# Optimization experiments

Hardware: AMD Instinct MI355X
Metric: run time of the kernel (lower is better)

Reference implementation:

```python
import jax, jax.numpy as jnp
import numpy as np

B, NV, NH = 65536, 16, 16


def _tri(key, b, n, scale=0.1):
    # well-conditioned lower-triangular 'cholesky-like' factor: unit diagonal + small strict-lower part
    a = jax.random.normal(key, (b, n, n), dtype=jnp.float32) * scale
    return jnp.tril(a, -1) + jnp.eye(n, dtype=jnp.float32)[None, :, :]


def setup_inputs() -> dict:
    key = jax.random.key(0)
    ks = jax.random.split(key, 9)
    # SPD, well-conditioned precision matrix for the hidden block
    a = jax.random.normal(ks[0], (B, NH, NH), dtype=jnp.float32)
    prec_h = jnp.eye(NH, dtype=jnp.float32)[None, :, :] + 0.1 * jnp.matmul(a, jnp.swapaxes(a, -1, -2)) / NH
    return {
        'mu_TE': jax.random.normal(ks[1], (B, NV + NH), dtype=jnp.float32),
        'prec_h': prec_h,
        'chol_v': _tri(ks[2], B, NV),
        'chol_h': _tri(ks[3], B, NH),
        'chol_hv': jax.random.normal(ks[4], (B, NH, NV), dtype=jnp.float32) * 0.1,
        'chol_v_TE': jax.random.normal(ks[5], (B, NV, NV), dtype=jnp.float32) * 0.1,
        'chol_h_TE': jax.random.normal(ks[6], (B, NH, NH), dtype=jnp.float32) * 0.1,
        'chol_hv_TE': jax.random.normal(ks[7], (B, NH, NV), dtype=jnp.float32) * 0.1,
        'chol_amat': _tri(ks[8], B, NV),
        'nv': NV,
    }


def reference(mu_TE, prec_h, chol_v, chol_h, chol_hv, chol_v_TE, chol_h_TE, chol_hv_TE, chol_amat, nv):
    T = lambda m: jnp.swapaxes(m, -1, -2)
    prec_h_inv = jnp.linalg.inv(prec_h)  # [B,nh,nh]

    # d/dt of prec_h_inv via product rule on chol factors
    sym = (chol_h_TE @ T(chol_h) + chol_h @ T(chol_h_TE)
           + chol_hv_TE @ T(chol_hv) + chol_hv @ T(chol_hv_TE))
    prec_h_inv_TE = -(prec_h_inv @ sym @ prec_h_inv)

    # amat_TE = -d/dt [ chol_hv^T prec_h_inv chol_hv ]  -> [B,nv,nv]
    amat_TE = -(T(chol_hv_TE) @ (prec_h_inv @ chol_hv)
                + T(chol_hv) @ (prec_h_inv_TE @ chol_hv)
                + T(chol_hv) @ (prec_h_inv @ chol_hv_TE))

    # make_chol_mat_TE: Phi(L^-1 A L^-T) keeps strict lower triangle + half diagonal
    n = chol_amat.shape[-1]
    phi_mask = jnp.tril(jnp.ones((n, n), jnp.float32), -1) + 0.5 * jnp.eye(n, dtype=jnp.float32)
    cinv = jnp.linalg.inv(chol_amat)
    arg = cinv @ amat_TE @ T(cinv)
    chol_amat_TE = chol_amat @ (arg * phi_mask)

    cholv_TE_std = chol_v_TE @ chol_amat + chol_v @ chol_amat_TE
    muv_TE = mu_TE[:, :nv]
    return cholv_TE_std, muv_TE
```

## Files before the change

kernel.cpp:

```cpp
#include <hip/hip_runtime.h>


typedef _Float16 h2 __attribute__((ext_vector_type(2)));

constexpr int PITCH = 20;
constexpr int IMG   = 8 * PITCH;
constexpr int NSLOT = 5;
constexpr int BSTR  = NSLOT * IMG + 8;

#define WBAR() __builtin_amdgcn_wave_barrier()

__device__ __forceinline__ unsigned int pkf(float a, float b) {
  return __builtin_bit_cast(unsigned int, __builtin_amdgcn_cvt_pkrtz(a, b));
}
__device__ __forceinline__ unsigned int h2add(unsigned int a, unsigned int b) {
  return __builtin_bit_cast(unsigned int,
      (h2)(__builtin_bit_cast(h2, a) + __builtin_bit_cast(h2, b)));
}
__device__ __forceinline__ float fd2(unsigned int a, unsigned int b, float c) {
#if __has_builtin(__builtin_amdgcn_fdot2)
  return __builtin_amdgcn_fdot2(__builtin_bit_cast(h2, a), __builtin_bit_cast(h2, b), c, false);
#else
  h2 ha = __builtin_bit_cast(h2, a), hb = __builtin_bit_cast(h2, b);
  return c + (float)ha.x * (float)hb.x + (float)ha.y * (float)hb.y;
#endif
}
__device__ __forceinline__ float dpp_swap1(float v) {
  return __int_as_float(__builtin_amdgcn_update_dpp(
      0, __float_as_int(v), 0xB1, 0xF, 0xF, false));
}

__device__ __forceinline__ void zero16(float (&v)[16]) {
  #pragma unroll
  for (int j = 0; j < 16; ++j) v[j] = 0.f;
}

__device__ __forceinline__ void ldtile(const float* __restrict__ g, size_t batch,
                                       int p, int q, float (&c)[16]) {
  const float* base = g + batch * 256 + p * 64 + q * 4;
  #pragma unroll
  for (int r = 0; r < 4; ++r) {
    float4 v = *reinterpret_cast<const float4*>(base + r * 16);
    c[r*4+0] = v.x; c[r*4+1] = v.y; c[r*4+2] = v.z; c[r*4+3] = v.w;
  }
}

__device__ __forceinline__ void storeRP(unsigned int* img, int p, int q, const float (&c)[16]) {
  #pragma unroll
  for (int r = 0; r < 4; ++r) {
    img[(2*q  ) * PITCH + 4*p + r] = pkf(c[r*4+0], c[r*4+1]);
    img[(2*q+1) * PITCH + 4*p + r] = pkf(c[r*4+2], c[r*4+3]);
  }
}
__device__ __forceinline__ void packCP(const float (&c)[16], unsigned int (&w)[8]) {
  w[0] = pkf(c[0],  c[4]);  w[1] = pkf(c[1],  c[5]);
  w[2] = pkf(c[2],  c[6]);  w[3] = pkf(c[3],  c[7]);
  w[4] = pkf(c[8],  c[12]); w[5] = pkf(c[9],  c[13]);
  w[6] = pkf(c[10], c[14]); w[7] = pkf(c[11], c[15]);
}
__device__ __forceinline__ void writeCPregs(unsigned int* img, int p, int q,
                                            const unsigned int (&w)[8]) {
  *reinterpret_cast<uint4*>(img + (2*p  ) * PITCH + 4*q) = make_uint4(w[0], w[1], w[2], w[3]);
  *reinterpret_cast<uint4*>(img + (2*p+1) * PITCH + 4*q) = make_uint4(w[4], w[5], w[6], w[7]);
}
__device__ __forceinline__ void storeCP(unsigned int* img, int p, int q, const float (&c)[16]) {
  unsigned int w[8];
  packCP(c, w);
  writeCPregs(img, p, q, w);
}

__device__ __forceinline__ void mm1(const unsigned int* __restrict__ A,
                                    const unsigned int* __restrict__ Bm,
                                    int p4, int q4, float (&c)[16]) {
  #pragma unroll
  for (int kp = 0; kp < 8; ++kp) {
    uint4 av = *reinterpret_cast<const uint4*>(A  + kp * PITCH + p4);
    uint4 bv = *reinterpret_cast<const uint4*>(Bm + kp * PITCH + q4);
    const unsigned int ar[4] = {av.x, av.y, av.z, av.w};
    const unsigned int br[4] = {bv.x, bv.y, bv.z, bv.w};
    #pragma unroll
    for (int r = 0; r < 4; ++r)
      #pragma unroll
      for (int j = 0; j < 4; ++j)
        c[r*4+j] = fd2(ar[r], br[j], c[r*4+j]);
  }
}
__device__ __forceinline__ void mm2(const unsigned int* __restrict__ A0,
                                    const unsigned int* __restrict__ A1,
                                    const unsigned int* __restrict__ Bm,
                                    int p4, int q4, float (&c)[16]) {
  #pragma unroll
  for (int kp = 0; kp < 8; ++kp) {
    uint4 a0 = *reinterpret_cast<const uint4*>(A0 + kp * PITCH + p4);
    uint4 a1 = *reinterpret_cast<const uint4*>(A1 + kp * PITCH + p4);
    uint4 bv = *reinterpret_cast<const uint4*>(Bm + kp * PITCH + q4);
    const unsigned int ar[4] = {h2add(a0.x, a1.x), h2add(a0.y, a1.y),
                                h2add(a0.z, a1.z), h2add(a0.w, a1.w)};
    const unsigned int br[4] = {bv.x, bv.y, bv.z, bv.w};
    #pragma unroll
    for (int r = 0; r < 4; ++r)
      #pragma unroll
      for (int j = 0; j < 4; ++j)
        c[r*4+j] = fd2(ar[r], br[j], c[r*4+j]);
  }
}

__global__ __launch_bounds__(64, 3) void gauss_te_pk5(
    const float* __restrict__ mu_TE,
    const float* __restrict__ prec_h,
    const float* __restrict__ chol_v,
    const float* __restrict__ chol_h,
    const float* __restrict__ chol_hv,
    const float* __restrict__ chol_v_TE,
    const float* __restrict__ chol_h_TE,
    const float* __restrict__ chol_hv_TE,
    const float* __restrict__ chol_amat,
    float* __restrict__ out, int B)
{
  __shared__ __align__(16) unsigned int slab[4 * BSTR];
  const int t = threadIdx.x;
  const int g = t >> 4;
  const int l = t & 15;
  const int p = l >> 2, q = l & 3;
  const int p4 = 4 * p, q4 = 4 * q;
  const size_t batch = (size_t)blockIdx.x * 4 + g;

  unsigned int* U = slab + g * BSTR;
  unsigned int* P0 = U;            unsigned int* P1 = U + 1*IMG;
  unsigned int* P2 = U + 2*IMG;    unsigned int* P3 = U + 3*IMG;
  unsigned int* P4 = U + 4*IMG;
  float* fcol = reinterpret_cast<float*>(P1);
  float* brow = fcol + 32;

  out[(size_t)B * 256 + batch * 16 + l] = mu_TE[batch * 32 + l];

  float tt[16];
  ldtile(chol_h, batch, p, q, tt);     storeRP(P0, p, q, tt);
  ldtile(chol_h_TE, batch, p, q, tt);  storeRP(P1, p, q, tt);
  unsigned int cphv[8], cphvT[8];
  ldtile(chol_hv, batch, p, q, tt);    storeRP(P2, p, q, tt);  packCP(tt, cphv);
  ldtile(chol_hv_TE, batch, p, q, tt); storeRP(P3, p, q, tt);  packCP(tt, cphvT);
  float pt[16];
  ldtile(prec_h, batch, p, q, pt);
  float la[16];
  ldtile(chol_amat, batch, p, q, la);
  WBAR();

  float c[16];

  zero16(c);
  mm1(P1, P0, p4, q4, c);
  mm1(P3, P2, p4, q4, c);
  storeCP(P4, c != nullptr ? p : p, q, c);
  WBAR();
  writeCPregs(P2, p, q, cphv);
  writeCPregs(P3, p, q, cphvT);
  WBAR();

  #pragma unroll
  for (int k = 0; k < 16; ++k) {
    const int kb = k >> 2, kc = k & 3, sel = (k & 1) * 16;
    if (q == kb) {
      *reinterpret_cast<float4*>(fcol + sel + p4) =
          make_float4(pt[0*4+kc], pt[1*4+kc], pt[2*4+kc], pt[3*4+kc]);
    }
    WBAR();
    if (p == kb) {
      const float rinv = 1.0f / fcol[sel + k];
      float sv[4];
      #pragma unroll
      for (int j = 0; j < 4; ++j) sv[j] = pt[kc*4+j] * rinv;
      if (q == kb) sv[kc] = rinv;
      *reinterpret_cast<float4*>(brow + sel + q4) = make_float4(sv[0], sv[1], sv[2], sv[3]);
    }
    WBAR();
    float4 f4 = *reinterpret_cast<const float4*>(fcol + sel + p4);
    float4 b4 = *reinterpret_cast<const float4*>(brow + sel + q4);
    const float fr[4] = {f4.x, f4.y, f4.z, f4.w};
    const float br[4] = {b4.x, b4.y, b4.z, b4.w};
    #pragma unroll
    for (int r = 0; r < 4; ++r) {
      const bool isPivRow = (p == kb) && (r == kc);
      #pragma unroll
      for (int j = 0; j < 4; ++j) {
        float base = pt[r*4+j];
        if (q == kb && j == kc) base = 0.f;
        const float nv = base - fr[r] * br[j];
        pt[r*4+j] = isPivRow ? br[j] : nv;
      }
    }
  }
  WBAR();
  storeRP(P0, p, q, pt);
  WBAR();

  zero16(c);
  mm1(P0, P4, p4, q4, c);
  WBAR();
  storeRP(P1, p, q, c);
  WBAR();

  zero16(c);
  mm1(P1, P0, p4, q4, c);
  WBAR();
  storeRP(P4, p, q, c);
  storeCP(P1, p, q, c);
  WBAR();

  zero16(c);
  mm1(P0, P2, p4, q4, c);
  WBAR();
  storeCP(P0, p, q, c);
  WBAR();

  zero16(c);
  mm2(P4, P1, P2, p4, q4, c);
  WBAR();
  storeCP(P4, p, q, c);
  WBAR();

  zero16(c);
  mm1(P3, P0, p4, q4, c);
  const int srcT = (t & 48) | ((t & 3) << 2) | ((t >> 2) & 3);
  float zsum[16];
  #pragma unroll
  for (int r = 0; r < 4; ++r)
    #pragma unroll
    for (int j = 0; j < 4; ++j)
      zsum[r*4+j] = c[r*4+j] + __shfl(c[j*4+r], srcT, 64);
  WBAR();

  zero16(c);
  mm1(P2, P4, p4, q4, c);
  #pragma unroll
  for (int j = 0; j < 16; ++j) c[j] -= zsum[j];
  WBAR();
  storeRP(P0, p, q, c);
  storeCP(P1, p, q, la);
  storeRP(P3, p, q, la);
  WBAR();

  float x[16];
  #pragma unroll
  for (int kp = 0; kp < 8; ++kp) {
    const int r0 = 2 * kp, r1 = r0 + 1;
    float a0 = 0.f, a1 = 0.f, h10 = 0.f;
    #pragma unroll
    for (int c2 = 0; c2 <= kp / 2; ++c2) {
      uint4 cv = *reinterpret_cast<const uint4*>(P1 + kp * PITCH + 4 * c2);
      const unsigned int cw[4] = {cv.x, cv.y, cv.z, cv.w};
      #pragma unroll
      for (int cc = 0; cc < 4; ++cc) {
        const int j = 4 * c2 + cc;
        h2 hp = __builtin_bit_cast(h2, cw[cc]);
        if (j < r0) a0 = fmaf(-(float)hp.x, x[j], a0);
        if (j < r0) a1 = fmaf(-(float)hp.y, x[j], a1);
        if (j == r0) h10 = (float)hp.y;
      }
    }
    x[r0] = ((l == r0) ? 1.f : 0.f) + a0;
    x[r1] = ((l == r1) ? 1.f : 0.f) + a1 - h10 * x[r0];
  }
  {
    float xp[16];
    #pragma unroll
    for (int j = 0; j < 16; ++j) xp[j] = dpp_swap1(x[j]);
    if ((l & 1) == 0) {
      unsigned int* dst = P2 + (l >> 1) * PITCH;
      #pragma unroll
      for (int c4 = 0; c4 < 4; ++c4) {
        uint4 w;
        w.x = pkf(x[4*c4+0], xp[4*c4+0]); w.y = pkf(x[4*c4+1], xp[4*c4+1]);
        w.z = pkf(x[4*c4+2], xp[4*c4+2]); w.w = pkf(x[4*c4+3], xp[4*c4+3]);
        *reinterpret_cast<uint4*>(dst + 4*c4) = w;
      }
    }
  }
  WBAR();

  float lvt[16], lv[16];
  ldtile(chol_v_TE, batch, p, q, lvt);
  ldtile(chol_v, batch, p, q, lv);

  zero16(c);
  mm1(P0, P2, p4, q4, c);
  WBAR();
  storeCP(P4, p, q, c);
  WBAR();

  zero16(c);
  mm1(P2, P4, p4, q4, c);
  #pragma unroll
  for (int r = 0; r < 4; ++r)
    #pragma unroll
    for (int j = 0; j < 4; ++j) {
      const int gi = p4 + r, gj = q4 + j;
      c[r*4+j] = (gi > gj) ? c[r*4+j] : ((gi == gj) ? 0.5f * c[r*4+j] : 0.f);
    }
  WBAR();
  storeCP(P0, p, q, c);
  WBAR();

  zero16(c);
  mm1(P3, P0, p4, q4, c);
  WBAR();
  storeCP(P4, p, q, c);
  storeRP(P0, p, q, lvt);
  storeRP(P2, p, q, lv);
  WBAR();

  zero16(c);
  mm1(P0, P1, p4, q4, c);
  mm1(P2, P4, p4, q4, c);
  {
    float* base = out + batch * 256 + p * 64 + q * 4;
    #pragma unroll
    for (int r = 0; r < 4; ++r)
      *reinterpret_cast<float4*>(base + r * 16) =
          make_float4(c[r*4+0], c[r*4+1], c[r*4+2], c[r*4+3]);
  }
}

extern "C" void kernel_launch(void* const* d_in, const int* in_sizes, int n_in,
                              void* d_out, int out_size, void* d_ws, size_t ws_size,
                              hipStream_t stream) {
  const float* mu_TE      = (const float*)d_in[0];
  const float* prec_h     = (const float*)d_in[1];
  const float* chol_v     = (const float*)d_in[2];
  const float* chol_h     = (const float*)d_in[3];
  const float* chol_hv    = (const float*)d_in[4];
  const float* chol_v_TE  = (const float*)d_in[5];
  const float* chol_h_TE  = (const float*)d_in[6];
  const float* chol_hv_TE = (const float*)d_in[7];
  const float* chol_amat  = (const float*)d_in[8];
  float* out = (float*)d_out;

  const int B = in_sizes[0] / 32;
  gauss_te_pk5<<<B / 4, 64, 0, stream>>>(mu_TE, prec_h, chol_v, chol_h, chol_hv,
                                         chol_v_TE, chol_h_TE, chol_hv_TE,
                                         chol_amat, out, B);
}
```

Before: 131.9 us.

## Replace fdot2 matrix products with 16x16x16 f16 MFMA across whole wave

The per-batch 16x16 matrix products, previously done by 16-lane groups with packed fdot2 on LDS images, now run as wave-wide 16x16x16 f16 MFMA instructions. Two batches are processed per pass, and several operands are loaded and converted straight from global memory. The algebra is also reassociated (P^-1 S P^-1, then a symmetric sum) so fewer LDS slots are needed. LDS per block shrinks from five slots to four and launch bounds rise to four blocks, aiming at higher occupancy and less ALU work, at the cost of more uncoalesced column loads and lane-layout shuffles.

```diff
diff --git a/kernel.cpp b/kernel.cpp
--- a/kernel.cpp
+++ b/kernel.cpp
@@ -1,38 +1,34 @@
 #include <hip/hip_runtime.h>
 
 
-typedef _Float16 h2 __attribute__((ext_vector_type(2)));
+typedef _Float16 h2    __attribute__((ext_vector_type(2)));
+typedef _Float16 f16x4 __attribute__((ext_vector_type(4)));
+typedef float    f32x4 __attribute__((ext_vector_type(4)));
 
 constexpr int PITCH = 20;
 constexpr int IMG   = 8 * PITCH;
-constexpr int NSLOT = 5;
-constexpr int BSTR  = NSLOT * IMG + 8;
+constexpr int BSTR  = 4 * IMG + 8;
 
 #define WBAR() __builtin_amdgcn_wave_barrier()
 
 __device__ __forceinline__ unsigned int pkf(float a, float b) {
   return __builtin_bit_cast(unsigned int, __builtin_amdgcn_cvt_pkrtz(a, b));
 }
-__device__ __forceinline__ unsigned int h2add(unsigned int a, unsigned int b) {
-  return __builtin_bit_cast(unsigned int,
-      (h2)(__builtin_bit_cast(h2, a) + __builtin_bit_cast(h2, b)));
-}
-__device__ __forceinline__ float fd2(unsigned int a, unsigned int b, float c) {
-#if __has_builtin(__builtin_amdgcn_fdot2)
-  return __builtin_amdgcn_fdot2(__builtin_bit_cast(h2, a), __builtin_bit_cast(h2, b), c, false);
-#else
-  h2 ha = __builtin_bit_cast(h2, a), hb = __builtin_bit_cast(h2, b);
-  return c + (float)ha.x * (float)hb.x + (float)ha.y * (float)hb.y;
-#endif
+__device__ __forceinline__ f16x4 mkf16x4(unsigned int lo, unsigned int hi) {
+  union { unsigned int u[2]; f16x4 v; } cv; cv.u[0] = lo; cv.u[1] = hi; return cv.v;
+}
+__device__ __forceinline__ f16x4 cvt4(f32x4 d) {
+  return mkf16x4(pkf(d[0], d[1]), pkf(d[2], d[3]));
+}
+__device__ __forceinline__ f16x4 cvt4f(float a, float b, float c, float d) {
+  return mkf16x4(pkf(a, b), pkf(c, d));
 }
 __device__ __forceinline__ float dpp_swap1(float v) {
   return __int_as_float(__builtin_amdgcn_update_dpp(
       0, __float_as_int(v), 0xB1, 0xF, 0xF, false));
 }
-
-__device__ __forceinline__ void zero16(float (&v)[16]) {
-  #pragma unroll
-  for (int j = 0; j < 16; ++j) v[j] = 0.f;
+__device__ __forceinline__ f32x4 MF(f16x4 a, f16x4 b, f32x4 c) {
+  return __builtin_amdgcn_mfma_f32_16x16x16f16(a, b, c, 0, 0, 0);
 }
 
 __device__ __forceinline__ void ldtile(const float* __restrict__ g, size_t batch,
@@ -44,7 +40,6 @@
     c[r*4+0] = v.x; c[r*4+1] = v.y; c[r*4+2] = v.z; c[r*4+3] = v.w;
   }
 }
-
 __device__ __forceinline__ void storeRP(unsigned int* img, int p, int q, const float (&c)[16]) {
   #pragma unroll
   for (int r = 0; r < 4; ++r) {
@@ -52,60 +47,39 @@
     img[(2*q+1) * PITCH + 4*p + r] = pkf(c[r*4+2], c[r*4+3]);
   }
 }
-__device__ __forceinline__ void packCP(const float (&c)[16], unsigned int (&w)[8]) {
-  w[0] = pkf(c[0],  c[4]);  w[1] = pkf(c[1],  c[5]);
-  w[2] = pkf(c[2],  c[6]);  w[3] = pkf(c[3],  c[7]);
-  w[4] = pkf(c[8],  c[12]); w[5] = pkf(c[9],  c[13]);
-  w[6] = pkf(c[10], c[14]); w[7] = pkf(c[11], c[15]);
-}
-__device__ __forceinline__ void writeCPregs(unsigned int* img, int p, int q,
-                                            const unsigned int (&w)[8]) {
-  *reinterpret_cast<uint4*>(img + (2*p  ) * PITCH + 4*q) = make_uint4(w[0], w[1], w[2], w[3]);
-  *reinterpret_cast<uint4*>(img + (2*p+1) * PITCH + 4*q) = make_uint4(w[4], w[5], w[6], w[7]);
-}
-__device__ __forceinline__ void storeCP(unsigned int* img, int p, int q, const float (&c)[16]) {
-  unsigned int w[8];
-  packCP(c, w);
-  writeCPregs(img, p, q, w);
-}
-
-__device__ __forceinline__ void mm1(const unsigned int* __restrict__ A,
-                                    const unsigned int* __restrict__ Bm,
-                                    int p4, int q4, float (&c)[16]) {
-  #pragma unroll
-  for (int kp = 0; kp < 8; ++kp) {
-    uint4 av = *reinterpret_cast<const uint4*>(A  + kp * PITCH + p4);
-    uint4 bv = *reinterpret_cast<const uint4*>(Bm + kp * PITCH + q4);
-    const unsigned int ar[4] = {av.x, av.y, av.z, av.w};
-    const unsigned int br[4] = {bv.x, bv.y, bv.z, bv.w};
-    #pragma unroll
-    for (int r = 0; r < 4; ++r)
-      #pragma unroll
-      for (int j = 0; j < 4; ++j)
-        c[r*4+j] = fd2(ar[r], br[j], c[r*4+j]);
-  }
-}
-__device__ __forceinline__ void mm2(const unsigned int* __restrict__ A0,
-                                    const unsigned int* __restrict__ A1,
-                                    const unsigned int* __restrict__ Bm,
-                                    int p4, int q4, float (&c)[16]) {
-  #pragma unroll
-  for (int kp = 0; kp < 8; ++kp) {
-    uint4 a0 = *reinterpret_cast<const uint4*>(A0 + kp * PITCH + p4);
-    uint4 a1 = *reinterpret_cast<const uint4*>(A1 + kp * PITCH + p4);
-    uint4 bv = *reinterpret_cast<const uint4*>(Bm + kp * PITCH + q4);
-    const unsigned int ar[4] = {h2add(a0.x, a1.x), h2add(a0.y, a1.y),
-                                h2add(a0.z, a1.z), h2add(a0.w, a1.w)};
-    const unsigned int br[4] = {bv.x, bv.y, bv.z, bv.w};
-    #pragma unroll
-    for (int r = 0; r < 4; ++r)
-      #pragma unroll
-      for (int j = 0; j < 4; ++j)
-        c[r*4+j] = fd2(ar[r], br[j], c[r*4+j]);
-  }
-}
-
-__global__ __launch_bounds__(64, 3) void gauss_te_pk5(
+__device__ __forceinline__ void storeCPt(unsigned int* img, int p, int q, const float (&c)[16]) {
+  uint4 w0, w1;
+  w0.x = pkf(c[0],  c[4]);  w0.y = pkf(c[1],  c[5]);
+  w0.z = pkf(c[2],  c[6]);  w0.w = pkf(c[3],  c[7]);
+  w1.x = pkf(c[8],  c[12]); w1.y = pkf(c[9],  c[13]);
+  w1.z = pkf(c[10], c[14]); w1.w = pkf(c[11], c[15]);
+  *reinterpret_cast<uint4*>(img + (2*p  ) * PITCH + 4*q) = w0;
+  *reinterpret_cast<uint4*>(img + (2*p+1) * PITCH + 4*q) = w1;
+}
+
+__device__ __forceinline__ f16x4 ldA(const float* __restrict__ X, int r, int h) {
+  float4 v = *reinterpret_cast<const float4*>(X + r * 16 + 4 * h);
+  return cvt4f(v.x, v.y, v.z, v.w);
+}
+__device__ __forceinline__ f16x4 ldBcol(const float* __restrict__ X, int h, int c) {
+  const float* b = X + 4 * h * 16 + c;
+  return cvt4f(b[0], b[16], b[32], b[48]);
+}
+__device__ __forceinline__ f16x4 ldsB(const unsigned int* img, int h, int c) {
+  return mkf16x4(img[(2*h) * PITCH + c], img[(2*h+1) * PITCH + c]);
+}
+__device__ __forceinline__ f16x4 ldsA(const unsigned int* img, int r, int h) {
+  uint4 u = *reinterpret_cast<const uint4*>(img + (r >> 1) * PITCH + 4 * h);
+  unsigned int sel = 0x05040100u + (unsigned)(r & 1) * 0x02020202u;
+  return mkf16x4(__builtin_amdgcn_perm(u.y, u.x, sel),
+                 __builtin_amdgcn_perm(u.w, u.z, sel));
+}
+__device__ __forceinline__ void stCP(unsigned int* img, int h, int c, f32x4 d) {
+  img[(2*h)   * PITCH + c] = pkf(d[0], d[1]);
+  img[(2*h+1) * PITCH + c] = pkf(d[2], d[3]);
+}
+
+__global__ __launch_bounds__(64, 4) void gauss_te_mf(
     const float* __restrict__ mu_TE,
     const float* __restrict__ prec_h,
     const float* __restrict__ chol_v,
@@ -122,46 +96,41 @@
   const int g = t >> 4;
   const int l = t & 15;
   const int p = l >> 2, q = l & 3;
-  const int p4 = 4 * p, q4 = 4 * q;
-  const size_t batch = (size_t)blockIdx.x * 4 + g;
-
-  unsigned int* U = slab + g * BSTR;
-  unsigned int* P0 = U;            unsigned int* P1 = U + 1*IMG;
-  unsigned int* P2 = U + 2*IMG;    unsigned int* P3 = U + 3*IMG;
-  unsigned int* P4 = U + 4*IMG;
-  float* fcol = reinterpret_cast<float*>(P1);
+  const size_t batch0 = (size_t)blockIdx.x * 4;
+  const size_t tb = batch0 + g;
+
+  unsigned int* Ut  = slab + g * BSTR;
+  unsigned int* Q0t = Ut;
+  unsigned int* Q1t = Ut + IMG;
+  unsigned int* Q2t = Ut + 2 * IMG;
+  unsigned int* Q3t = Ut + 3 * IMG;
+  float* fcol = reinterpret_cast<float*>(Q3t);
   float* brow = fcol + 32;
 
-  out[(size_t)B * 256 + batch * 16 + l] = mu_TE[batch * 32 + l];
-
-  float tt[16];
-  ldtile(chol_h, batch, p, q, tt);     storeRP(P0, p, q, tt);
-  ldtile(chol_h_TE, batch, p, q, tt);  storeRP(P1, p, q, tt);
-  unsigned int cphv[8], cphvT[8];
-  ldtile(chol_hv, batch, p, q, tt);    storeRP(P2, p, q, tt);  packCP(tt, cphv);
-  ldtile(chol_hv_TE, batch, p, q, tt); storeRP(P3, p, q, tt);  packCP(tt, cphvT);
+  out[(size_t)B * 256 + tb * 16 + l] = mu_TE[tb * 32 + l];
+
+  f16x4 pfA0[4], pfB0[4], pfA1[4], pfB1[4];
+  #pragma unroll
+  for (int b = 0; b < 4; ++b) {
+    const size_t off = (batch0 + b) * 256;
+    pfA0[b] = ldA(chol_h_TE  + off, l, g);
+    pfB0[b] = ldA(chol_h     + off, l, g);
+    pfA1[b] = ldA(chol_hv_TE + off, l, g);
+    pfB1[b] = ldA(chol_hv    + off, l, g);
+  }
+
+  float la[16];
+  ldtile(chol_amat, tb, p, q, la);
+  storeCPt(Q1t, p, q, la);
   float pt[16];
-  ldtile(prec_h, batch, p, q, pt);
-  float la[16];
-  ldtile(chol_amat, batch, p, q, la);
-  WBAR();
-
-  float c[16];
-
-  zero16(c);
-  mm1(P1, P0, p4, q4, c);
-  mm1(P3, P2, p4, q4, c);
-  storeCP(P4, c != nullptr ? p : p, q, c);
-  WBAR();
-  writeCPregs(P2, p, q, cphv);
-  writeCPregs(P3, p, q, cphvT);
+  ldtile(prec_h, tb, p, q, pt);
   WBAR();
 
   #pragma unroll
   for (int k = 0; k < 16; ++k) {
     const int kb = k >> 2, kc = k & 3, sel = (k & 1) * 16;
     if (q == kb) {
-      *reinterpret_cast<float4*>(fcol + sel + p4) =
+      *reinterpret_cast<float4*>(fcol + sel + 4 * p) =
           make_float4(pt[0*4+kc], pt[1*4+kc], pt[2*4+kc], pt[3*4+kc]);
     }
     WBAR();
@@ -171,11 +140,11 @@
       #pragma unroll
       for (int j = 0; j < 4; ++j) sv[j] = pt[kc*4+j] * rinv;
       if (q == kb) sv[kc] = rinv;
-      *reinterpret_cast<float4*>(brow + sel + q4) = make_float4(sv[0], sv[1], sv[2], sv[3]);
-    }
-    WBAR();
-    float4 f4 = *reinterpret_cast<const float4*>(fcol + sel + p4);
-    float4 b4 = *reinterpret_cast<const float4*>(brow + sel + q4);
+      *reinterpret_cast<float4*>(brow + sel + 4 * q) = make_float4(sv[0], sv[1], sv[2], sv[3]);
+    }
+    WBAR();
+    float4 f4 = *reinterpret_cast<const float4*>(fcol + sel + 4 * p);
+    float4 b4 = *reinterpret_cast<const float4*>(brow + sel + 4 * q);
     const float fr[4] = {f4.x, f4.y, f4.z, f4.w};
     const float br[4] = {b4.x, b4.y, b4.z, b4.w};
     #pragma unroll
@@ -191,53 +160,7 @@
     }
   }
   WBAR();
-  storeRP(P0, p, q, pt);
-  WBAR();
-
-  zero16(c);
-  mm1(P0, P4, p4, q4, c);
-  WBAR();
-  storeRP(P1, p, q, c);
-  WBAR();
-
-  zero16(c);
-  mm1(P1, P0, p4, q4, c);
-  WBAR();
-  storeRP(P4, p, q, c);
-  storeCP(P1, p, q, c);
-  WBAR();
-
-  zero16(c);
-  mm1(P0, P2, p4, q4, c);
-  WBAR();
-  storeCP(P0, p, q, c);
-  WBAR();
-
-  zero16(c);
-  mm2(P4, P1, P2, p4, q4, c);
-  WBAR();
-  storeCP(P4, p, q, c);
-  WBAR();
-
-  zero16(c);
-  mm1(P3, P0, p4, q4, c);
-  const int srcT = (t & 48) | ((t & 3) << 2) | ((t >> 2) & 3);
-  float zsum[16];
-  #pragma unroll
-  for (int r = 0; r < 4; ++r)
-    #pragma unroll
-    for (int j = 0; j < 4; ++j)
-      zsum[r*4+j] = c[r*4+j] + __shfl(c[j*4+r], srcT, 64);
-  WBAR();
-
-  zero16(c);
-  mm1(P2, P4, p4, q4, c);
-  #pragma unroll
-  for (int j = 0; j < 16; ++j) c[j] -= zsum[j];
-  WBAR();
-  storeRP(P0, p, q, c);
-  storeCP(P1, p, q, la);
-  storeRP(P3, p, q, la);
+  storeRP(Q0t, p, q, pt);
   WBAR();
 
   float x[16];
@@ -247,7 +170,7 @@
     float a0 = 0.f, a1 = 0.f, h10 = 0.f;
     #pragma unroll
     for (int c2 = 0; c2 <= kp / 2; ++c2) {
-      uint4 cv = *reinterpret_cast<const uint4*>(P1 + kp * PITCH + 4 * c2);
+      uint4 cv = *reinterpret_cast<const uint4*>(Q1t + kp * PITCH + 4 * c2);
       const unsigned int cw[4] = {cv.x, cv.y, cv.z, cv.w};
       #pragma unroll
       for (int cc = 0; cc < 4; ++cc) {
@@ -266,7 +189,7 @@
     #pragma unroll
     for (int j = 0; j < 16; ++j) xp[j] = dpp_swap1(x[j]);
     if ((l & 1) == 0) {
-      unsigned int* dst = P2 + (l >> 1) * PITCH;
+      unsigned int* dst = Q2t + (l >> 1) * PITCH;
       #pragma unroll
       for (int c4 = 0; c4 < 4; ++c4) {
         uint4 w;
@@ -278,46 +201,82 @@
   }
   WBAR();
 
-  float lvt[16], lv[16];
-  ldtile(chol_v_TE, batch, p, q, lvt);
-  ldtile(chol_v, batch, p, q, lv);
-
-  zero16(c);
-  mm1(P0, P2, p4, q4, c);
-  WBAR();
-  storeCP(P4, p, q, c);
-  WBAR();
-
-  zero16(c);
-  mm1(P2, P4, p4, q4, c);
-  #pragma unroll
-  for (int r = 0; r < 4; ++r)
-    #pragma unroll
-    for (int j = 0; j < 4; ++j) {
-      const int gi = p4 + r, gj = q4 + j;
-      c[r*4+j] = (gi > gj) ? c[r*4+j] : ((gi == gj) ? 0.5f * c[r*4+j] : 0.f);
-    }
-  WBAR();
-  storeCP(P0, p, q, c);
-  WBAR();
-
-  zero16(c);
-  mm1(P3, P0, p4, q4, c);
-  WBAR();
-  storeCP(P4, p, q, c);
-  storeRP(P0, p, q, lvt);
-  storeRP(P2, p, q, lv);
-  WBAR();
-
-  zero16(c);
-  mm1(P0, P1, p4, q4, c);
-  mm1(P2, P4, p4, q4, c);
-  {
-    float* base = out + batch * 256 + p * 64 + q * 4;
-    #pragma unroll
-    for (int r = 0; r < 4; ++r)
-      *reinterpret_cast<float4*>(base + r * 16) =
-          make_float4(c[r*4+0], c[r*4+1], c[r*4+2], c[r*4+3]);
+  const f32x4 zz = {0.f, 0.f, 0.f, 0.f};
+  #pragma unroll
+  for (int gb = 0; gb < 4; gb += 2) {
+    const unsigned int* Q0[2] = { slab + (gb+0)*BSTR, slab + (gb+1)*BSTR };
+    const unsigned int* Q1[2] = { Q0[0] + IMG,        Q0[1] + IMG };
+    const unsigned int* Q2[2] = { Q0[0] + 2*IMG,      Q0[1] + 2*IMG };
+    unsigned int*       Q3[2] = { slab + (gb+0)*BSTR + 3*IMG,
+                                  slab + (gb+1)*BSTR + 3*IMG };
+    const size_t off[2] = { (batch0 + gb + 0) * 256, (batch0 + gb + 1) * 256 };
+
+    f16x4 pinvA[2], pinvB[2], hvB[2], cA[2], sumA[2];
+    f32x4 W[2], M1[2], Up[2], Zt[2], V2[2];
+
+    #pragma unroll
+    for (int u = 0; u < 2; ++u) {
+      f32x4 S = MF(pfA0[gb+u], pfB0[gb+u], zz);
+      S = MF(pfA1[gb+u], pfB1[gb+u], S);
+      pinvA[u] = ldsA(Q0[u], l, g);
+      pinvB[u] = ldsB(Q0[u], g, l);
+      f32x4 W1 = MF(pinvA[u], cvt4(S), zz);
+      stCP(Q3[u], g, l, W1);
+    }
+    WBAR();
+    #pragma unroll
+    for (int u = 0; u < 2; ++u) {
+      f16x4 w1A = ldsA(Q3[u], l, g);
+      W[u] = MF(w1A, pinvB[u], zz);
+    }
+    #pragma unroll
+    for (int u = 0; u < 2; ++u) stCP(Q3[u], g, l, W[u]);
+    WBAR();
+    #pragma unroll
+    for (int u = 0; u < 2; ++u) {
+      f16x4 wA = ldsA(Q3[u], l, g);
+      sumA[u] = wA + cvt4(W[u]);
+      hvB[u] = ldBcol(chol_hv + off[u], g, l);
+      M1[u] = MF(pinvA[u], hvB[u], zz);
+      Up[u] = MF(sumA[u], hvB[u], zz);
+    }
+    #pragma unroll
+    for (int u = 0; u < 2; ++u) {
+      f16x4 hvtB = ldBcol(chol_hv_TE + off[u], g, l);
+      Zt[u] = MF(hvtB, cvt4(M1[u]), zz);
+      V2[u] = MF(hvB[u], cvt4(Up[u]), zz);
+      stCP(Q3[u], g, l, Zt[u]);
+    }
+    WBAR();
+    f32x4 T1[2];
+    #pragma unroll
+    for (int u = 0; u < 2; ++u) {
+      f16x4 zA = ldsA(Q3[u], l, g);
+      f32x4 am = V2[u] - Zt[u];
+      am[0] -= (float)zA[0]; am[1] -= (float)zA[1];
+      am[2] -= (float)zA[2]; am[3] -= (float)zA[3];
+      cA[u] = ldsB(Q2[u], g, l);
+      T1[u] = MF(cA[u], cvt4(am), zz);
+      stCP(Q3[u], g, l, T1[u]);
+    }
+    WBAR();
+    #pragma unroll
+    for (int u = 0; u < 2; ++u) {
+      f16x4 t1A = ldsA(Q3[u], l, g);
+      f32x4 arg = MF(t1A, cA[u], zz);
+      #pragma unroll
+      for (int j = 0; j < 4; ++j) {
+        const int r = 4 * g + j;
+        arg[j] = (r > l) ? arg[j] : ((r == l) ? 0.5f * arg[j] : 0.f);
+      }
+      f32x4 cam = MF(ldA(chol_amat + off[u], l, g), cvt4(arg), zz);
+      f16x4 laB = ldsB(Q1[u], g, l);
+      f32x4 ov = MF(ldA(chol_v_TE + off[u], l, g), laB, zz);
+      ov = MF(ldA(chol_v + off[u], l, g), cvt4(cam), ov);
+      float* ob = out + off[u];
+      #pragma unroll
+      for (int j = 0; j < 4; ++j) ob[(4 * g + j) * 16 + l] = ov[j];
+    }
   }
 }
 
@@ -336,7 +295,7 @@
   float* out = (float*)d_out;
 
   const int B = in_sizes[0] / 32;
-  gauss_te_pk5<<<B / 4, 64, 0, stream>>>(mu_TE, prec_h, chol_v, chol_h, chol_hv,
-                                         chol_v_TE, chol_h_TE, chol_hv_TE,
-                                         chol_amat, out, B);
-}
+  gauss_te_mf<<<B / 4, 64, 0, stream>>>(mu_TE, prec_h, chol_v, chol_h, chol_hv,
+                                        chol_v_TE, chol_h_TE, chol_hv_TE,
+                                        chol_amat, out, B);
+}
```

Measured after the change: 126.6 us. 1.04x faster.
